# Performance work log

Hardware: AMD Instinct MI355X
Metric: run time of the kernel (lower is better)

Reference implementation:

```python
import jax, jax.numpy as jnp
import numpy as np

N, M, D_IN = 2048, 2048, 16
INV_SP_13 = float(np.log(np.expm1(1.3)))  # invsoftplus(1.3), lengthscale init
INV_SP_05 = float(np.log(np.expm1(0.5)))  # invsoftplus(0.5), variance init


def setup_inputs() -> dict:
    key = jax.random.key(0)
    k1, k2 = jax.random.split(key)
    X = jax.random.normal(k1, (N, D_IN), dtype=jnp.float32)
    X2 = jax.random.normal(k2, (M, D_IN), dtype=jnp.float32)
    uls = jnp.full((D_IN,), INV_SP_13, dtype=jnp.float32)  # unconstrained lengthscales
    uv = jnp.full((1,), INV_SP_05, dtype=jnp.float32)      # unconstrained variance
    return {"X": X, "X2": X2, "uls": uls, "uv": uv}


def reference(X, X2, uls, uv):
    D_in = X.shape[1]
    ls = jax.nn.softplus(uls)          # (D,)
    var = jax.nn.softplus(uv)          # (1,)
    Xl = X / ls                        # (N, D)
    X2l = X2 / ls                      # (M, D)
    Xs = jnp.sum(Xl * Xl, axis=1)      # (N,)
    X2s = jnp.sum(X2l * X2l, axis=1)   # (M,)
    # scaled squared distance (N, M)
    sq_dist = -2.0 * (Xl @ X2l.T) + Xs[:, None] + X2s[None, :]
    K2 = jnp.exp(-0.5 * sq_dist)       # (N, M)
    # K1_term[d,n,m] = diff[n,m,d]^2 ; keep layout (N, M, D)
    diff = Xl[:, None, :] - X2l[None, :, :]           # (N, M, D)
    K1 = diff * diff                                   # (N, M, D)
    K3 = (D_in - 1.0 - sq_dist)                        # (N, M); @ identity is a no-op
    K = (K1 + K3[:, :, None]) * K2[:, :, None]         # (N, M, D)
    l2 = 1.0 / (ls * ls)                               # (D,)
    out = (K @ l2) * var[0]                            # (N, M)
    return out
```

## Files before the change

### kernel.cpp

```cpp
#include <hip/hip_runtime.h>
#include <math.h>

constexpr int N_ROWS = 2048;
constexpr int M_COLS = 2048;
constexpr int D = 16;

constexpr int BM = 256;
constexpr int BN = 32;

__global__ __launch_bounds__(256, 4) void dfk_kernel(
    const float* __restrict__ X, const float* __restrict__ X2,
    const float* __restrict__ uls, const float* __restrict__ uv,
    float* __restrict__ out) {
  __shared__ float sh_par[2 * D + 1];
  __shared__ float shX[BN * D];
  __shared__ float shS[BN * 2];

  const int tid = threadIdx.x;
  const int m = blockIdx.x * BM + tid;
  const int n0 = blockIdx.y * BN;

  if (tid <= D) {
    const float u = (tid < D) ? uls[tid] : uv[0];
    const float sp = fmaxf(u, 0.f) + log1pf(__expf(-fabsf(u)));
    if (tid < D) {
      const float il = 1.f / sp;
      sh_par[tid] = il;
      sh_par[D + tid] = il * il;
    } else {
      sh_par[2 * D] = sp;
    }
  }
  __syncthreads();

  float inv_ls[D], w[D];
  float wsum = 0.f;
#pragma unroll
  for (int d = 0; d < D; ++d) {
    inv_ls[d] = sh_par[d];
    w[d] = sh_par[D + d];
    wsum += w[d];
  }
  const float var = sh_par[2 * D];

  if (tid < BN) {
    const float* xr = X + (size_t)(n0 + tid) * D;
    float xs = 0.f, xw = 0.f;
#pragma unroll
    for (int q = 0; q < 4; ++q) {
      float4 v = ((const float4*)xr)[q];
      v.x *= inv_ls[q * 4 + 0];
      v.y *= inv_ls[q * 4 + 1];
      v.z *= inv_ls[q * 4 + 2];
      v.w *= inv_ls[q * 4 + 3];
      xs += v.x * v.x + v.y * v.y + v.z * v.z + v.w * v.w;
      xw += v.x * v.x * w[q * 4 + 0] + v.y * v.y * w[q * 4 + 1] +
            v.z * v.z * w[q * 4 + 2] + v.w * v.w * w[q * 4 + 3];
      ((float4*)(shX + tid * D))[q] = v;
    }
    shS[tid * 2 + 0] = xs;
    shS[tid * 2 + 1] = xw;
  }

  float x2l[D], x2lw[D];
  float X2s = 0.f, X2w = 0.f;
#pragma unroll
  for (int q = 0; q < 4; ++q) {
    float4 v = ((const float4*)(X2 + (size_t)m * D))[q];
#pragma unroll
    for (int j = 0; j < 4; ++j) {
      const int d = q * 4 + j;
      const float e = (&v.x)[j] * inv_ls[d];
      x2l[d] = e;
      x2lw[d] = e * w[d];
      X2s += e * e;
      X2w += e * e * w[d];
    }
  }
  __syncthreads();

  const float c3 = (float)D - 1.0f;
#pragma unroll 2
  for (int i = 0; i < BN; ++i) {
    const float4* row = (const float4*)(shX + i * D);
    float dot = 0.f, dotw = 0.f;
#pragma unroll
    for (int q = 0; q < 4; ++q) {
      float4 v = row[q];
      dot = fmaf(v.x, x2l[q * 4 + 0], dot);
      dot = fmaf(v.y, x2l[q * 4 + 1], dot);
      dot = fmaf(v.z, x2l[q * 4 + 2], dot);
      dot = fmaf(v.w, x2l[q * 4 + 3], dot);
      dotw = fmaf(v.x, x2lw[q * 4 + 0], dotw);
      dotw = fmaf(v.y, x2lw[q * 4 + 1], dotw);
      dotw = fmaf(v.z, x2lw[q * 4 + 2], dotw);
      dotw = fmaf(v.w, x2lw[q * 4 + 3], dotw);
    }
    const float sq = shS[i * 2 + 0] + X2s - 2.f * dot;
    const float S = shS[i * 2 + 1] + X2w - 2.f * dotw;
    const float k2 = __expf(-0.5f * sq);
    const float res = var * k2 * fmaf(c3 - sq, wsum, S);
    out[(size_t)(n0 + i) * M_COLS + m] = res;
  }
}

extern "C" void kernel_launch(void* const* d_in, const int* in_sizes, int n_in,
                              void* d_out, int out_size, void* d_ws, size_t ws_size,
                              hipStream_t stream) {
  const float* X = (const float*)d_in[0];
  const float* X2 = (const float*)d_in[1];
  const float* uls = (const float*)d_in[2];
  const float* uv = (const float*)d_in[3];
  float* out = (float*)d_out;

  dim3 grid(M_COLS / BM, N_ROWS / BN);
  dfk_kernel<<<grid, dim3(BM), 0, stream>>>(X, X2, uls, uv, out);
}
```

Baseline: 70.69 us.

## Fold lengthscale scaling into X2 side, use packed FMA, read X rows directly

```diff
diff --git a/kernel.cpp b/kernel.cpp
--- a/kernel.cpp
+++ b/kernel.cpp
@@ -6,15 +6,23 @@
 constexpr int D = 16;
 
 constexpr int BM = 256;
-constexpr int BN = 32;
+constexpr int BN = 16;
+
+typedef float f2 __attribute__((ext_vector_type(2)));
+
+static __device__ __forceinline__ f2 mk2(float a, float b) {
+  f2 r;
+  r.x = a;
+  r.y = b;
+  return r;
+}
 
 __global__ __launch_bounds__(256, 4) void dfk_kernel(
     const float* __restrict__ X, const float* __restrict__ X2,
     const float* __restrict__ uls, const float* __restrict__ uv,
     float* __restrict__ out) {
-  __shared__ float sh_par[2 * D + 1];
-  __shared__ float shX[BN * D];
-  __shared__ float shS[BN * 2];
+  __shared__ __align__(16) float sh_w[D + 1];
+  __shared__ float2 shS[BN];
 
   const int tid = threadIdx.x;
   const int m = blockIdx.x * BM + tid;
@@ -25,81 +33,120 @@
     const float sp = fmaxf(u, 0.f) + log1pf(__expf(-fabsf(u)));
     if (tid < D) {
       const float il = 1.f / sp;
-      sh_par[tid] = il;
-      sh_par[D + tid] = il * il;
+      sh_w[tid] = il * il;
     } else {
-      sh_par[2 * D] = sp;
+      sh_w[D] = sp;
     }
   }
   __syncthreads();
 
-  float inv_ls[D], w[D];
+  float w[D];
   float wsum = 0.f;
 #pragma unroll
-  for (int d = 0; d < D; ++d) {
-    inv_ls[d] = sh_par[d];
-    w[d] = sh_par[D + d];
-    wsum += w[d];
+  for (int q = 0; q < 4; ++q) {
+    const float4 wq = ((const float4*)sh_w)[q];
+    w[4 * q + 0] = wq.x;
+    w[4 * q + 1] = wq.y;
+    w[4 * q + 2] = wq.z;
+    w[4 * q + 3] = wq.w;
+    wsum += wq.x + wq.y + wq.z + wq.w;
   }
-  const float var = sh_par[2 * D];
+  const float var = sh_w[D];
+
+  f2 a2[8], a2w[8];
+  float X2s = 0.f, X2w = 0.f;
+  {
+    const float4* x2r = (const float4*)(X2 + (size_t)m * D);
+#pragma unroll
+    for (int q = 0; q < 4; ++q) {
+      const float4 v = x2r[q];
+      const float a0 = v.x * w[4 * q + 0];
+      const float a1 = v.y * w[4 * q + 1];
+      const float b0 = v.z * w[4 * q + 2];
+      const float b1 = v.w * w[4 * q + 3];
+      X2s = fmaf(v.x, a0, X2s);
+      X2s = fmaf(v.y, a1, X2s);
+      X2s = fmaf(v.z, b0, X2s);
+      X2s = fmaf(v.w, b1, X2s);
+      X2w = fmaf(a0, a0, X2w);
+      X2w = fmaf(a1, a1, X2w);
+      X2w = fmaf(b0, b0, X2w);
+      X2w = fmaf(b1, b1, X2w);
+      a2[2 * q + 0] = mk2(a0, a1);
+      a2[2 * q + 1] = mk2(b0, b1);
+      a2w[2 * q + 0] = mk2(a0 * w[4 * q + 0], a1 * w[4 * q + 1]);
+      a2w[2 * q + 1] = mk2(b0 * w[4 * q + 2], b1 * w[4 * q + 3]);
+    }
+  }
 
   if (tid < BN) {
-    const float* xr = X + (size_t)(n0 + tid) * D;
+    const float4* xr = (const float4*)(X + (size_t)(n0 + tid) * D);
     float xs = 0.f, xw = 0.f;
 #pragma unroll
     for (int q = 0; q < 4; ++q) {
-      float4 v = ((const float4*)xr)[q];
-      v.x *= inv_ls[q * 4 + 0];
-      v.y *= inv_ls[q * 4 + 1];
-      v.z *= inv_ls[q * 4 + 2];
-      v.w *= inv_ls[q * 4 + 3];
-      xs += v.x * v.x + v.y * v.y + v.z * v.z + v.w * v.w;
-      xw += v.x * v.x * w[q * 4 + 0] + v.y * v.y * w[q * 4 + 1] +
-            v.z * v.z * w[q * 4 + 2] + v.w * v.w * w[q * 4 + 3];
-      ((float4*)(shX + tid * D))[q] = v;
+      const float4 v = xr[q];
+      const float t0 = v.x * v.x;
+      const float t1 = v.y * v.y;
+      const float t2 = v.z * v.z;
+      const float t3 = v.w * v.w;
+      xs = fmaf(t0, w[4 * q + 0], xs);
+      xs = fmaf(t1, w[4 * q + 1], xs);
+      xs = fmaf(t2, w[4 * q + 2], xs);
+      xs = fmaf(t3, w[4 * q + 3], xs);
+      xw = fmaf(t0, w[4 * q + 0] * w[4 * q + 0], xw);
+      xw = fmaf(t1, w[4 * q + 1] * w[4 * q + 1], xw);
+      xw = fmaf(t2, w[4 * q + 2] * w[4 * q + 2], xw);
+      xw = fmaf(t3, w[4 * q + 3] * w[4 * q + 3], xw);
     }
-    shS[tid * 2 + 0] = xs;
-    shS[tid * 2 + 1] = xw;
-  }
-
-  float x2l[D], x2lw[D];
-  float X2s = 0.f, X2w = 0.f;
-#pragma unroll
-  for (int q = 0; q < 4; ++q) {
-    float4 v = ((const float4*)(X2 + (size_t)m * D))[q];
-#pragma unroll
-    for (int j = 0; j < 4; ++j) {
-      const int d = q * 4 + j;
-      const float e = (&v.x)[j] * inv_ls[d];
-      x2l[d] = e;
-      x2lw[d] = e * w[d];
-      X2s += e * e;
-      X2w += e * e * w[d];
-    }
+    shS[tid] = make_float2(xs, xw);
   }
   __syncthreads();
 
-  const float c3 = (float)D - 1.0f;
-#pragma unroll 2
+  const float cS = ((float)D - 1.f) * wsum;
+
+#pragma unroll 4
   for (int i = 0; i < BN; ++i) {
-    const float4* row = (const float4*)(shX + i * D);
-    float dot = 0.f, dotw = 0.f;
-#pragma unroll
-    for (int q = 0; q < 4; ++q) {
-      float4 v = row[q];
-      dot = fmaf(v.x, x2l[q * 4 + 0], dot);
-      dot = fmaf(v.y, x2l[q * 4 + 1], dot);
-      dot = fmaf(v.z, x2l[q * 4 + 2], dot);
-      dot = fmaf(v.w, x2l[q * 4 + 3], dot);
-      dotw = fmaf(v.x, x2lw[q * 4 + 0], dotw);
-      dotw = fmaf(v.y, x2lw[q * 4 + 1], dotw);
-      dotw = fmaf(v.z, x2lw[q * 4 + 2], dotw);
-      dotw = fmaf(v.w, x2lw[q * 4 + 3], dotw);
-    }
-    const float sq = shS[i * 2 + 0] + X2s - 2.f * dot;
-    const float S = shS[i * 2 + 1] + X2w - 2.f * dotw;
+    const float4* xr = (const float4*)(X + (size_t)(n0 + i) * D);
+    const float4 r0 = xr[0];
+    const float4 r1 = xr[1];
+    const float4 r2 = xr[2];
+    const float4 r3 = xr[3];
+
+    f2 acc = mk2(0.f, 0.f);
+    f2 accw = mk2(0.f, 0.f);
+    f2 s;
+    s = mk2(r0.x, r0.y);
+    acc = __builtin_elementwise_fma(s, a2[0], acc);
+    accw = __builtin_elementwise_fma(s, a2w[0], accw);
+    s = mk2(r0.z, r0.w);
+    acc = __builtin_elementwise_fma(s, a2[1], acc);
+    accw = __builtin_elementwise_fma(s, a2w[1], accw);
+    s = mk2(r1.x, r1.y);
+    acc = __builtin_elementwise_fma(s, a2[2], acc);
+    accw = __builtin_elementwise_fma(s, a2w[2], accw);
+    s = mk2(r1.z, r1.w);
+    acc = __builtin_elementwise_fma(s, a2[3], acc);
+    accw = __builtin_elementwise_fma(s, a2w[3], accw);
+    s = mk2(r2.x, r2.y);
+    acc = __builtin_elementwise_fma(s, a2[4], acc);
+    accw = __builtin_elementwise_fma(s, a2w[4], accw);
+    s = mk2(r2.z, r2.w);
+    acc = __builtin_elementwise_fma(s, a2[5], acc);
+    accw = __builtin_elementwise_fma(s, a2w[5], accw);
+    s = mk2(r3.x, r3.y);
+    acc = __builtin_elementwise_fma(s, a2[6], acc);
+    accw = __builtin_elementwise_fma(s, a2w[6], accw);
+    s = mk2(r3.z, r3.w);
+    acc = __builtin_elementwise_fma(s, a2[7], acc);
+    accw = __builtin_elementwise_fma(s, a2w[7], accw);
+
+    const float dot = acc.x + acc.y;
+    const float dotw = accw.x + accw.y;
+    const float2 xsxw = shS[i];
+    const float sq = fmaf(-2.f, dot, xsxw.x + X2s);
+    const float S = fmaf(-2.f, dotw, xsxw.y + X2w);
     const float k2 = __expf(-0.5f * sq);
-    const float res = var * k2 * fmaf(c3 - sq, wsum, S);
+    const float res = var * k2 * fmaf(-wsum, sq, cS + S);
     out[(size_t)(n0 + i) * M_COLS + m] = res;
   }
 }
```

New measurement: 70.77 us. No clear change (+0.1%).
